# Kernel optimization log

Hardware: AMD Instinct MI355X
Metric: run time of the kernel (lower is better)

## Reference

```python
import jax, jax.numpy as jnp
import numpy as np

B, S, D, H = 16, 512, 512, 8
DH = D // H
EPS = 1e-5
NEG = -1.0e9


def _layernorm(v, g, b):
    mu = jnp.mean(v, axis=-1, keepdims=True)
    var = jnp.mean(jnp.square(v - mu), axis=-1, keepdims=True)
    return (v - mu) * jax.lax.rsqrt(var + EPS) * g + b


def setup_inputs() -> dict:
    key = jax.random.key(0)
    ks = jax.random.split(key, 12)
    sd = 1.0 / np.sqrt(D)
    return {
        "x": jax.random.normal(ks[0], (B, S, D), dtype=jnp.float32),
        "mask": jax.random.randint(ks[1], (B, S, S), 0, 2, dtype=jnp.int32),
        "ln_g": jnp.ones((D,), jnp.float32),
        "ln_b": jnp.zeros((D,), jnp.float32),
        "lna_g": jnp.ones((S,), jnp.float32),  # LayerNorm over attention scores (last dim = S = model_dim)
        "lna_b": jnp.zeros((S,), jnp.float32),
        "Wq": jax.random.uniform(ks[2], (D, D), jnp.float32, -sd, sd),
        "bq": jnp.zeros((D,), jnp.float32),
        "Wk": jax.random.uniform(ks[3], (D, D), jnp.float32, -sd, sd),
        "bk": jnp.zeros((D,), jnp.float32),
        "Wv": jax.random.uniform(ks[4], (D, D), jnp.float32, -sd, sd),
        "bv": jnp.zeros((D,), jnp.float32),
        "Wd": jax.random.uniform(ks[5], (D, D), jnp.float32, -sd, sd),
        "bd": jnp.zeros((D,), jnp.float32),
    }


def reference(x, mask, ln_g, ln_b, lna_g, lna_b, Wq, bq, Wk, bk, Wv, bv, Wd, bd):
    # pre-LN
    h = _layernorm(x, ln_g, ln_b)  # [B,S,D]
    # projections -> [B,H,S,DH]
    q = (h @ Wq + bq).reshape(B, S, H, DH).transpose(0, 2, 1, 3)
    k = (h @ Wk + bk).reshape(B, S, H, DH).transpose(0, 2, 1, 3)
    v = (h @ Wv + bv).reshape(B, S, H, DH).transpose(0, 2, 1, 3)
    # raw scores [B,H,S,S]
    scores = jnp.einsum("bhqd,bhkd->bhqk", q, k) / jnp.sqrt(jnp.asarray(DH, x.dtype))
    # non-standard: LayerNorm over the key axis of the score matrix
    scores = _layernorm(scores, lna_g, lna_b)
    # mask (broadcast over heads), then softmax
    scores = jnp.where(mask[:, None, :, :] == 0, jnp.asarray(NEG, x.dtype), scores)
    attn = jax.nn.softmax(scores, axis=-1)
    # dropout omitted (eval mode / deterministic reference)
    out = jnp.einsum("bhqk,bhkd->bhqd", attn, v)
    out = out.transpose(0, 2, 1, 3).reshape(B, S, D)
    out = out @ Wd + bd
    return out + x
```

## Files before the change

### kernel.cpp

```cpp
#include <hip/hip_runtime.h>
#include <hip/hip_bf16.h>
#include <stdint.h>


typedef __hip_bfloat16 bf16;
typedef __bf16 bf16x8 __attribute__((ext_vector_type(8)));
typedef float f32x4 __attribute__((ext_vector_type(4)));

#define MFMA16(a, b, c) __builtin_amdgcn_mfma_f32_16x16x32_bf16((a), (b), (c), 0, 0, 0)

static __device__ __forceinline__ bf16 f2b(float v) { return __float2bfloat16(v); }
static __device__ __forceinline__ bf16x8 ld8(const bf16* p) { return *(const bf16x8*)p; }
static __device__ __forceinline__ uint16_t f2bu(float v) {
  return __hip_bfloat16_raw(__float2bfloat16(v)).x;
}
static __device__ __forceinline__ float bu2f(uint32_t u) {
  union { uint32_t i; float f; } c;
  c.i = u << 16;
  return c.f;
}

__global__ __launch_bounds__(256) void transpose512(
    const float* __restrict__ W0, const float* __restrict__ W1,
    const float* __restrict__ W2, const float* __restrict__ W3,
    bf16* __restrict__ T0, bf16* __restrict__ T1,
    bf16* __restrict__ T2, bf16* __restrict__ T3) {
  __shared__ float t[32][33];
  const float* src; bf16* dst;
  switch (blockIdx.z) {
    case 0: src = W0; dst = T0; break;
    case 1: src = W1; dst = T1; break;
    case 2: src = W2; dst = T2; break;
    default: src = W3; dst = T3; break;
  }
  int tx = threadIdx.x, ty = threadIdx.y;
  int n0 = blockIdx.x * 32, k0 = blockIdx.y * 32;
#pragma unroll
  for (int i = 0; i < 4; i++) {
    int kk = ty * 4 + i;
    t[kk][tx] = src[(k0 + kk) * 512 + n0 + tx];
  }
  __syncthreads();
#pragma unroll
  for (int i = 0; i < 4; i++) {
    int nn = ty * 4 + i;
    dst[(n0 + nn) * 512 + k0 + tx] = f2b(t[tx][nn]);
  }
}

__global__ __launch_bounds__(256) void mask_pack(const int* __restrict__ mask,
                                                 uint32_t* __restrict__ bits) {
  size_t t = (size_t)blockIdx.x * 256 + threadIdx.x;
  int mv = mask[t];
  unsigned long long bal = __ballot(mv != 0);
  if ((threadIdx.x & 63) == 0) {
    ((unsigned long long*)bits)[t >> 6] = bal;
  }
}

__global__ __launch_bounds__(256) void mask_transpose(const uint32_t* __restrict__ bits,
                                                      uint32_t* __restrict__ tbits) {
  int t = blockIdx.x * 256 + threadIdx.x;
  int row = t >> 4, l = t & 15;
  const uint32_t* in = bits + row * 16;
  uint32_t o = 0;
#pragma unroll
  for (int jj = 0; jj < 32; jj++) {
    int key = l + 16 * jj;
    o |= ((in[key >> 5] >> (key & 31)) & 1u) << jj;
  }
  tbits[t] = o;
}

__global__ __launch_bounds__(256) void ln_rows(
    const float* __restrict__ x, const float* __restrict__ g,
    const float* __restrict__ be, bf16* __restrict__ h) {
  int row = blockIdx.x;
  int tid = threadIdx.x;
  const float* xr = x + (size_t)row * 512;
  float v0 = xr[tid], v1 = xr[tid + 256];
  float s = v0 + v1, s2 = v0 * v0 + v1 * v1;
#pragma unroll
  for (int m = 1; m < 64; m <<= 1) {
    s += __shfl_xor(s, m);
    s2 += __shfl_xor(s2, m);
  }
  __shared__ float rs[4], rs2[4];
  int w = tid >> 6;
  if ((tid & 63) == 0) { rs[w] = s; rs2[w] = s2; }
  __syncthreads();
  s = rs[0] + rs[1] + rs[2] + rs[3];
  s2 = rs2[0] + rs2[1] + rs2[2] + rs2[3];
  float mean = s * (1.0f / 512.0f);
  float var = s2 * (1.0f / 512.0f) - mean * mean;
  float rstd = rsqrtf(var + 1e-5f);
  bf16* hr = h + (size_t)row * 512;
  hr[tid] = f2b((v0 - mean) * rstd * g[tid] + be[tid]);
  hr[tid + 256] = f2b((v1 - mean) * rstd * g[tid + 256] + be[tid + 256]);
}

__global__ __launch_bounds__(256) void gemm_qkv(
    const bf16* __restrict__ hm,
    const bf16* __restrict__ WT0, const bf16* __restrict__ WT1, const bf16* __restrict__ WT2,
    const float* __restrict__ bq, const float* __restrict__ bk, const float* __restrict__ bv,
    bf16* __restrict__ outq, bf16* __restrict__ outk, bf16* __restrict__ outvT) {
  const int sel = blockIdx.z;
  const bf16* WT = sel == 0 ? WT0 : (sel == 1 ? WT1 : WT2);
  const float* bias = sel == 0 ? bq : (sel == 1 ? bk : bv);
  __shared__ __align__(16) bf16 As[128][40];
  __shared__ __align__(16) bf16 Bs[128][40];
  int tid = threadIdx.x;
  int w = tid >> 6, lane = tid & 63, q4 = lane >> 4, l16 = lane & 15;
  int wr = w >> 1, wc = w & 1;
  int m0 = blockIdx.x * 128, n0 = blockIdx.y * 128;
  f32x4 acc[4][4];
#pragma unroll
  for (int i = 0; i < 4; i++)
#pragma unroll
    for (int j = 0; j < 4; j++) acc[i][j] = (f32x4){0.f, 0.f, 0.f, 0.f};

  for (int kc = 0; kc < 16; kc++) {
    int k0 = kc * 32;
#pragma unroll
    for (int u = tid; u < 512; u += 256) {
      int row = u >> 2, c8 = (u & 3) * 8;
      *(bf16x8*)&As[row][c8] = ld8(&hm[(size_t)(m0 + row) * 512 + k0 + c8]);
      *(bf16x8*)&Bs[row][c8] = ld8(&WT[(size_t)(n0 + row) * 512 + k0 + c8]);
    }
    __syncthreads();
    bf16x8 af[4], bfr[4];
#pragma unroll
    for (int rt = 0; rt < 4; rt++) af[rt] = ld8(&As[wr * 64 + rt * 16 + l16][q4 * 8]);
#pragma unroll
    for (int nt = 0; nt < 4; nt++) bfr[nt] = ld8(&Bs[wc * 64 + nt * 16 + l16][q4 * 8]);
#pragma unroll
    for (int rt = 0; rt < 4; rt++)
#pragma unroll
      for (int nt = 0; nt < 4; nt++) acc[rt][nt] = MFMA16(af[rt], bfr[nt], acc[rt][nt]);
    __syncthreads();
  }

#pragma unroll
  for (int rt = 0; rt < 4; rt++) {
    int mbase = m0 + wr * 64 + rt * 16 + q4 * 4;
    int b = mbase >> 9, s0 = mbase & 511;
#pragma unroll
    for (int nt = 0; nt < 4; nt++) {
      int n = n0 + wc * 64 + nt * 16 + l16;
      float bsv = bias[n];
      int hh = n >> 6, dh = n & 63;
      if (sel == 2) {
        union { bf16 q[4]; uint2 u; } pk;
#pragma unroll
        for (int r = 0; r < 4; r++) pk.q[r] = f2b(acc[rt][nt][r] + bsv);
        *(uint2*)(outvT + ((size_t)((b * 8 + hh) * 64 + dh)) * 512 + s0) = pk.u;
      } else {
        bf16* dst = sel == 0 ? outq : outk;
        float scale = sel == 0 ? 0.125f : 1.0f;
#pragma unroll
        for (int r = 0; r < 4; r++)
          dst[((size_t)((b * 8 + hh) * 512 + s0 + r)) * 64 + dh] =
              f2b((acc[rt][nt][r] + bsv) * scale);
      }
    }
  }
}

__global__ __launch_bounds__(256, 2) void attn_fused(
    const bf16* __restrict__ q, const bf16* __restrict__ k, const bf16* __restrict__ vT,
    const uint32_t* __restrict__ tbits, const float* __restrict__ lg,
    const float* __restrict__ lb, bf16* __restrict__ ctx) {
  const int id = blockIdx.x;
  const int xcd = id & 7;
  const int j = id >> 3;
  const int mt = j & 7;
  const int bh = ((j >> 3) << 3) | xcd;
  const int m0 = mt * 64;
  const int b = bh >> 3, hh = bh & 7;
  const int tid = threadIdx.x;
  const int w = tid >> 6, lane = tid & 63, q4 = lane >> 4, l16 = lane & 15;

  __shared__ uint16_t ST[512][66];
  __shared__ __align__(16) bf16 SB[2][2560];

  const bf16* qb = q + ((size_t)bh * 512 + m0 + w * 16) * 64;
  const bf16* kb = k + (size_t)bh * 512 * 64;
  const bf16* vb = vT + (size_t)bh * 64 * 512;

  bf16x8 aq0 = ld8(qb + (size_t)l16 * 64 + q4 * 8);
  bf16x8 aq1 = ld8(qb + (size_t)l16 * 64 + 32 + q4 * 8);

  uint32_t tb[4];
#pragma unroll
  for (int r = 0; r < 4; r++)
    tb[r] = tbits[((size_t)b * 512 + m0 + w * 16 + q4 * 4 + r) * 16 + l16];

  const int col = w * 16 + q4 * 4;

  {
    int key0 = tid >> 3, dh8 = (tid & 7) * 8;
    *(bf16x8*)&SB[0][key0 * 72 + dh8] = ld8(kb + (size_t)key0 * 64 + dh8);
  }
  __syncthreads();

  float s[4] = {0.f, 0.f, 0.f, 0.f}, s2[4] = {0.f, 0.f, 0.f, 0.f};
  for (int c = 0; c < 16; c++) {
    const int buf = c & 1;
    if (c < 15) {
      int key0 = tid >> 3, dh8 = (tid & 7) * 8;
      *(bf16x8*)&SB[buf ^ 1][key0 * 72 + dh8] =
          ld8(kb + (size_t)((c + 1) * 32 + key0) * 64 + dh8);
    }
#pragma unroll
    for (int kg = 0; kg < 2; kg++) {
      const bf16* kp = &SB[buf][(kg * 16 + l16) * 72];
      bf16x8 b0 = ld8(kp + q4 * 8);
      bf16x8 b1 = ld8(kp + 32 + q4 * 8);
      f32x4 acc = (f32x4){0.f, 0.f, 0.f, 0.f};
      acc = MFMA16(aq0, b0, acc);
      acc = MFMA16(aq1, b1, acc);
#pragma unroll
      for (int r = 0; r < 4; r++) {
        float v = acc[r];
        s[r] += v;
        s2[r] += v * v;
      }
      int key = c * 32 + kg * 16 + l16;
      *(uint32_t*)&ST[key][col] = (uint32_t)f2bu(acc[0]) | ((uint32_t)f2bu(acc[1]) << 16);
      *(uint32_t*)&ST[key][col + 2] = (uint32_t)f2bu(acc[2]) | ((uint32_t)f2bu(acc[3]) << 16);
    }
    __syncthreads();
  }

  float mean[4], rstd[4];
#pragma unroll
  for (int r = 0; r < 4; r++) {
    float a = s[r], a2 = s2[r];
#pragma unroll
    for (int mm = 1; mm < 16; mm <<= 1) {
      a += __shfl_xor(a, mm);
      a2 += __shfl_xor(a2, mm);
    }
    float mu = a * (1.0f / 512.0f);
    float var = a2 * (1.0f / 512.0f) - mu * mu;
    mean[r] = mu;
    rstd[r] = rsqrtf(var + 1e-5f);
  }

  float se[4] = {0.f, 0.f, 0.f, 0.f};
#pragma unroll
  for (int i = 0; i < 32; i++) {
    int key = i * 16 + l16;
    float g = lg[key], be = lb[key];
    uint32_t d0 = *(uint32_t*)&ST[key][col];
    uint32_t d1 = *(uint32_t*)&ST[key][col + 2];
    float v[4] = {bu2f(d0 & 0xffff), bu2f(d0 >> 16), bu2f(d1 & 0xffff), bu2f(d1 >> 16)};
    uint16_t p[4];
#pragma unroll
    for (int r = 0; r < 4; r++) {
      float t = (v[r] - mean[r]) * rstd[r] * g + be;
      t = ((tb[r] >> i) & 1u) ? t : -1.0e9f;
      float pf = __expf(t);
      se[r] += pf;
      p[r] = f2bu(pf);
    }
    *(uint32_t*)&ST[key][col] = (uint32_t)p[0] | ((uint32_t)p[1] << 16);
    *(uint32_t*)&ST[key][col + 2] = (uint32_t)p[2] | ((uint32_t)p[3] << 16);
  }
  float inv[4];
#pragma unroll
  for (int r = 0; r < 4; r++) {
    float a = se[r];
#pragma unroll
    for (int mm = 1; mm < 16; mm <<= 1) a += __shfl_xor(a, mm);
    inv[r] = 1.0f / a;
  }

  {
    int dh = tid >> 2, kk8 = (tid & 3) * 8;
    *(bf16x8*)&SB[0][dh * 40 + kk8] = ld8(vb + (size_t)dh * 512 + kk8);
  }
  __syncthreads();

  f32x4 o[4];
#pragma unroll
  for (int nt = 0; nt < 4; nt++) o[nt] = (f32x4){0.f, 0.f, 0.f, 0.f};

  for (int c = 0; c < 16; c++) {
    const int buf = c & 1;
    if (c < 15) {
      int dh = tid >> 2, kk8 = (tid & 3) * 8;
      *(bf16x8*)&SB[buf ^ 1][dh * 40 + kk8] =
          ld8(vb + (size_t)dh * 512 + (c + 1) * 32 + kk8);
    }
    union { uint16_t u[8]; bf16x8 v; } af;
#pragma unroll
    for (int jj = 0; jj < 8; jj++) af.u[jj] = ST[c * 32 + q4 * 8 + jj][w * 16 + l16];
#pragma unroll
    for (int nt = 0; nt < 4; nt++) {
      bf16x8 bv8 = ld8(&SB[buf][(nt * 16 + l16) * 40 + q4 * 8]);
      o[nt] = MFMA16(af.v, bv8, o[nt]);
    }
    __syncthreads();
  }

  bf16* cb = ctx + ((size_t)b * 512 + m0 + w * 16) * 512 + hh * 64;
#pragma unroll
  for (int nt = 0; nt < 4; nt++)
#pragma unroll
    for (int r = 0; r < 4; r++)
      cb[(size_t)(q4 * 4 + r) * 512 + nt * 16 + l16] = f2b(o[nt][r] * inv[r]);
}

__global__ __launch_bounds__(256) void gemm_out(
    const bf16* __restrict__ ctx, const bf16* __restrict__ WT,
    const float* __restrict__ bd, const float* __restrict__ x, float* __restrict__ out) {
  __shared__ __align__(16) bf16 As[128][40];
  __shared__ __align__(16) bf16 Bs[128][40];
  int tid = threadIdx.x;
  int w = tid >> 6, lane = tid & 63, q4 = lane >> 4, l16 = lane & 15;
  int wr = w >> 1, wc = w & 1;
  int m0 = blockIdx.x * 128, n0 = blockIdx.y * 128;
  f32x4 acc[4][4];
#pragma unroll
  for (int i = 0; i < 4; i++)
#pragma unroll
    for (int j = 0; j < 4; j++) acc[i][j] = (f32x4){0.f, 0.f, 0.f, 0.f};

  for (int kc = 0; kc < 16; kc++) {
    int k0 = kc * 32;
#pragma unroll
    for (int u = tid; u < 512; u += 256) {
      int row = u >> 2, c8 = (u & 3) * 8;
      *(bf16x8*)&As[row][c8] = ld8(&ctx[(size_t)(m0 + row) * 512 + k0 + c8]);
      *(bf16x8*)&Bs[row][c8] = ld8(&WT[(size_t)(n0 + row) * 512 + k0 + c8]);
    }
    __syncthreads();
    bf16x8 af[4], bfr[4];
#pragma unroll
    for (int rt = 0; rt < 4; rt++) af[rt] = ld8(&As[wr * 64 + rt * 16 + l16][q4 * 8]);
#pragma unroll
    for (int nt = 0; nt < 4; nt++) bfr[nt] = ld8(&Bs[wc * 64 + nt * 16 + l16][q4 * 8]);
#pragma unroll
    for (int rt = 0; rt < 4; rt++)
#pragma unroll
      for (int nt = 0; nt < 4; nt++) acc[rt][nt] = MFMA16(af[rt], bfr[nt], acc[rt][nt]);
    __syncthreads();
  }
#pragma unroll
  for (int rt = 0; rt < 4; rt++) {
    int mbase = m0 + wr * 64 + rt * 16 + q4 * 4;
#pragma unroll
    for (int nt = 0; nt < 4; nt++) {
      int n = n0 + wc * 64 + nt * 16 + l16;
      float bsv = bd[n];
#pragma unroll
      for (int r = 0; r < 4; r++) {
        size_t idx = (size_t)(mbase + r) * 512 + n;
        out[idx] = acc[rt][nt][r] + bsv + x[idx];
      }
    }
  }
}

extern "C" void kernel_launch(void* const* d_in, const int* in_sizes, int n_in,
                              void* d_out, int out_size, void* d_ws, size_t ws_size,
                              hipStream_t stream) {
  const float* x = (const float*)d_in[0];
  const int* mask = (const int*)d_in[1];
  const float* ln_g = (const float*)d_in[2];
  const float* ln_b = (const float*)d_in[3];
  const float* lna_g = (const float*)d_in[4];
  const float* lna_b = (const float*)d_in[5];
  const float* Wq = (const float*)d_in[6];
  const float* bq = (const float*)d_in[7];
  const float* Wk = (const float*)d_in[8];
  const float* bk = (const float*)d_in[9];
  const float* Wv = (const float*)d_in[10];
  const float* bv = (const float*)d_in[11];
  const float* Wd = (const float*)d_in[12];
  const float* bd = (const float*)d_in[13];

  char* ws = (char*)d_ws;
  const size_t MB = 1024 * 1024;
  if (ws_size < 44 * MB) return;
  bf16* h = (bf16*)(ws);
  bf16* qd = (bf16*)(ws + 8 * MB);
  bf16* kd = (bf16*)(ws + 16 * MB);
  bf16* vTd = (bf16*)(ws + 24 * MB);
  bf16* ctx = (bf16*)(ws + 32 * MB);
  bf16* WqT = (bf16*)(ws + 40 * MB);
  bf16* WkT = (bf16*)(ws + 40 * MB + 512 * 1024);
  bf16* WvT = (bf16*)(ws + 40 * MB + 1024 * 1024);
  bf16* WdT = (bf16*)(ws + 40 * MB + 1536 * 1024);
  uint32_t* bits = (uint32_t*)(ws + 42 * MB);
  uint32_t* tbits = (uint32_t*)(ws + 42 * MB + 512 * 1024);

  transpose512<<<dim3(16, 16, 4), dim3(32, 8), 0, stream>>>(Wq, Wk, Wv, Wd, WqT, WkT, WvT, WdT);
  mask_pack<<<16384, 256, 0, stream>>>(mask, bits);
  mask_transpose<<<512, 256, 0, stream>>>(bits, tbits);
  ln_rows<<<8192, 256, 0, stream>>>(x, ln_g, ln_b, h);
  gemm_qkv<<<dim3(64, 4, 3), 256, 0, stream>>>(h, WqT, WkT, WvT, bq, bk, bv, qd, kd, vTd);
  attn_fused<<<1024, 256, 0, stream>>>(qd, kd, vTd, tbits, lna_g, lna_b, ctx);
  gemm_out<<<dim3(64, 4), 256, 0, stream>>>(ctx, WdT, bd, x, (float*)d_out);
}
```

Measured before the change: 205.0 us.

## Keep attention score tile in registers and shrink LDS to raise occupancy

The 512x64 bf16 score tile no longer lives in shared memory. Each thread now keeps its share of scores in 64 packed registers across the QK, LayerNorm/softmax and PV phases. For the PV MFMA, the A operand is transposed through a small per-wave scratch buffer guarded only by compiler fences. The LayerNorm gamma and beta vectors are staged in LDS, and the occupancy hint is raised to 3 blocks per CU. This removes most LDS traffic and footprint, but raises register pressure and risks spills. It also relies on intra-wave ordering of LDS accesses without a barrier.

```diff
diff --git a/kernel.cpp b/kernel.cpp
--- a/kernel.cpp
+++ b/kernel.cpp
@@ -8,6 +8,7 @@
 typedef float f32x4 __attribute__((ext_vector_type(4)));
 
 #define MFMA16(a, b, c) __builtin_amdgcn_mfma_f32_16x16x32_bf16((a), (b), (c), 0, 0, 0)
+#define WAVE_LDS_FENCE() asm volatile("" ::: "memory")
 
 static __device__ __forceinline__ bf16 f2b(float v) { return __float2bfloat16(v); }
 static __device__ __forceinline__ bf16x8 ld8(const bf16* p) { return *(const bf16x8*)p; }
@@ -166,7 +167,7 @@
   }
 }
 
-__global__ __launch_bounds__(256, 2) void attn_fused(
+__global__ __launch_bounds__(256, 3) void attn_fused(
     const bf16* __restrict__ q, const bf16* __restrict__ k, const bf16* __restrict__ vT,
     const uint32_t* __restrict__ tbits, const float* __restrict__ lg,
     const float* __restrict__ lb, bf16* __restrict__ ctx) {
@@ -180,8 +181,14 @@
   const int tid = threadIdx.x;
   const int w = tid >> 6, lane = tid & 63, q4 = lane >> 4, l16 = lane & 15;
 
-  __shared__ uint16_t ST[512][66];
   __shared__ __align__(16) bf16 SB[2][2560];
+  __shared__ uint16_t PBT[4][32][18];
+  __shared__ float SG[512], SBt[512];
+
+  SG[tid] = lg[tid];
+  SG[tid + 256] = lg[tid + 256];
+  SBt[tid] = lb[tid];
+  SBt[tid + 256] = lb[tid + 256];
 
   const bf16* qb = q + ((size_t)bh * 512 + m0 + w * 16) * 64;
   const bf16* kb = k + (size_t)bh * 512 * 64;
@@ -195,15 +202,15 @@
   for (int r = 0; r < 4; r++)
     tb[r] = tbits[((size_t)b * 512 + m0 + w * 16 + q4 * 4 + r) * 16 + l16];
 
-  const int col = w * 16 + q4 * 4;
-
   {
     int key0 = tid >> 3, dh8 = (tid & 7) * 8;
     *(bf16x8*)&SB[0][key0 * 72 + dh8] = ld8(kb + (size_t)key0 * 64 + dh8);
   }
   __syncthreads();
 
+  uint32_t sc[64];
   float s[4] = {0.f, 0.f, 0.f, 0.f}, s2[4] = {0.f, 0.f, 0.f, 0.f};
+#pragma unroll
   for (int c = 0; c < 16; c++) {
     const int buf = c & 1;
     if (c < 15) {
@@ -225,9 +232,8 @@
         s[r] += v;
         s2[r] += v * v;
       }
-      int key = c * 32 + kg * 16 + l16;
-      *(uint32_t*)&ST[key][col] = (uint32_t)f2bu(acc[0]) | ((uint32_t)f2bu(acc[1]) << 16);
-      *(uint32_t*)&ST[key][col + 2] = (uint32_t)f2bu(acc[2]) | ((uint32_t)f2bu(acc[3]) << 16);
+      sc[c * 4 + kg * 2] = (uint32_t)f2bu(acc[0]) | ((uint32_t)f2bu(acc[1]) << 16);
+      sc[c * 4 + kg * 2 + 1] = (uint32_t)f2bu(acc[2]) | ((uint32_t)f2bu(acc[3]) << 16);
     }
     __syncthreads();
   }
@@ -249,24 +255,26 @@
 
   float se[4] = {0.f, 0.f, 0.f, 0.f};
 #pragma unroll
-  for (int i = 0; i < 32; i++) {
-    int key = i * 16 + l16;
-    float g = lg[key], be = lb[key];
-    uint32_t d0 = *(uint32_t*)&ST[key][col];
-    uint32_t d1 = *(uint32_t*)&ST[key][col + 2];
-    float v[4] = {bu2f(d0 & 0xffff), bu2f(d0 >> 16), bu2f(d1 & 0xffff), bu2f(d1 >> 16)};
-    uint16_t p[4];
-#pragma unroll
-    for (int r = 0; r < 4; r++) {
-      float t = (v[r] - mean[r]) * rstd[r] * g + be;
-      t = ((tb[r] >> i) & 1u) ? t : -1.0e9f;
-      float pf = __expf(t);
-      se[r] += pf;
-      p[r] = f2bu(pf);
-    }
-    *(uint32_t*)&ST[key][col] = (uint32_t)p[0] | ((uint32_t)p[1] << 16);
-    *(uint32_t*)&ST[key][col + 2] = (uint32_t)p[2] | ((uint32_t)p[3] << 16);
-  }
+  for (int c = 0; c < 16; c++)
+#pragma unroll
+    for (int kg = 0; kg < 2; kg++) {
+      int key = c * 32 + kg * 16 + l16;
+      float g = SG[key], be = SBt[key];
+      int bit = 2 * c + kg;
+      uint32_t d0 = sc[c * 4 + kg * 2], d1 = sc[c * 4 + kg * 2 + 1];
+      float v[4] = {bu2f(d0 & 0xffff), bu2f(d0 >> 16), bu2f(d1 & 0xffff), bu2f(d1 >> 16)};
+      uint16_t p[4];
+#pragma unroll
+      for (int r = 0; r < 4; r++) {
+        float t = (v[r] - mean[r]) * rstd[r] * g + be;
+        t = ((tb[r] >> bit) & 1u) ? t : -1.0e9f;
+        float pf = __expf(t);
+        se[r] += pf;
+        p[r] = f2bu(pf);
+      }
+      sc[c * 4 + kg * 2] = (uint32_t)p[0] | ((uint32_t)p[1] << 16);
+      sc[c * 4 + kg * 2 + 1] = (uint32_t)p[2] | ((uint32_t)p[3] << 16);
+    }
   float inv[4];
 #pragma unroll
   for (int r = 0; r < 4; r++) {
@@ -286,6 +294,7 @@
 #pragma unroll
   for (int nt = 0; nt < 4; nt++) o[nt] = (f32x4){0.f, 0.f, 0.f, 0.f};
 
+#pragma unroll
   for (int c = 0; c < 16; c++) {
     const int buf = c & 1;
     if (c < 15) {
@@ -293,9 +302,15 @@
       *(bf16x8*)&SB[buf ^ 1][dh * 40 + kk8] =
           ld8(vb + (size_t)dh * 512 + (c + 1) * 32 + kk8);
     }
+    *(uint32_t*)&PBT[w][l16][q4 * 4] = sc[c * 4 + 0];
+    *(uint32_t*)&PBT[w][l16][q4 * 4 + 2] = sc[c * 4 + 1];
+    *(uint32_t*)&PBT[w][16 + l16][q4 * 4] = sc[c * 4 + 2];
+    *(uint32_t*)&PBT[w][16 + l16][q4 * 4 + 2] = sc[c * 4 + 3];
+    WAVE_LDS_FENCE();
     union { uint16_t u[8]; bf16x8 v; } af;
 #pragma unroll
-    for (int jj = 0; jj < 8; jj++) af.u[jj] = ST[c * 32 + q4 * 8 + jj][w * 16 + l16];
+    for (int jj = 0; jj < 8; jj++) af.u[jj] = PBT[w][q4 * 8 + jj][l16];
+    WAVE_LDS_FENCE();
 #pragma unroll
     for (int nt = 0; nt < 4; nt++) {
       bf16x8 bv8 = ld8(&SB[buf][(nt * 16 + l16) * 40 + q4 * 8]);
```

Result: slower. 233.4 us (+13.9%).

## Fuse mask packing into one kernel and stage GEMM tiles via direct global-to-LDS loads

Applied to the files above, without the earlier changes.

Merges the mask ballot-pack and bit-transpose kernels into a single kernel that reads the int mask directly and emits transposed bit words, removing one launch and an intermediate buffer. The QKV and output GEMMs now fill LDS with global_load_lds (direct global-to-LDS) instead of load-to-register then store, and drop the padded 40-column LDS rows for unpadded 32-column rows. The unpadded layout may bring back LDS bank conflicts on fragment reads. The new mask kernel uses a strided access pattern with only 512 blocks, which may coalesce poorly over the 16MB mask.

```diff
diff --git a/kernel.cpp b/kernel.cpp
--- a/kernel.cpp
+++ b/kernel.cpp
@@ -18,6 +18,11 @@
   union { uint32_t i; float f; } c;
   c.i = u << 16;
   return c.f;
+}
+static __device__ __forceinline__ void stage16(const bf16* g, bf16* l) {
+  __builtin_amdgcn_global_load_lds(
+      (const __attribute__((address_space(1))) void*)g,
+      (__attribute__((address_space(3))) void*)l, 16, 0, 0);
 }
 
 __global__ __launch_bounds__(256) void transpose512(
@@ -48,27 +53,14 @@
   }
 }
 
-__global__ __launch_bounds__(256) void mask_pack(const int* __restrict__ mask,
-                                                 uint32_t* __restrict__ bits) {
-  size_t t = (size_t)blockIdx.x * 256 + threadIdx.x;
-  int mv = mask[t];
-  unsigned long long bal = __ballot(mv != 0);
-  if ((threadIdx.x & 63) == 0) {
-    ((unsigned long long*)bits)[t >> 6] = bal;
-  }
-}
-
-__global__ __launch_bounds__(256) void mask_transpose(const uint32_t* __restrict__ bits,
-                                                      uint32_t* __restrict__ tbits) {
+__global__ __launch_bounds__(256) void mask_bits(const int* __restrict__ mask,
+                                                 uint32_t* __restrict__ tbits) {
   int t = blockIdx.x * 256 + threadIdx.x;
   int row = t >> 4, l = t & 15;
-  const uint32_t* in = bits + row * 16;
+  const int* mrow = mask + (size_t)row * 512 + l;
   uint32_t o = 0;
 #pragma unroll
-  for (int jj = 0; jj < 32; jj++) {
-    int key = l + 16 * jj;
-    o |= ((in[key >> 5] >> (key & 31)) & 1u) << jj;
-  }
+  for (int j = 0; j < 32; j++) o |= (mrow[j * 16] != 0 ? 1u : 0u) << j;
   tbits[t] = o;
 }
 
@@ -107,8 +99,8 @@
   const int sel = blockIdx.z;
   const bf16* WT = sel == 0 ? WT0 : (sel == 1 ? WT1 : WT2);
   const float* bias = sel == 0 ? bq : (sel == 1 ? bk : bv);
-  __shared__ __align__(16) bf16 As[128][40];
-  __shared__ __align__(16) bf16 Bs[128][40];
+  __shared__ __align__(16) bf16 As[128 * 32];
+  __shared__ __align__(16) bf16 Bs[128 * 32];
   int tid = threadIdx.x;
   int w = tid >> 6, lane = tid & 63, q4 = lane >> 4, l16 = lane & 15;
   int wr = w >> 1, wc = w & 1;
@@ -122,17 +114,20 @@
   for (int kc = 0; kc < 16; kc++) {
     int k0 = kc * 32;
 #pragma unroll
-    for (int u = tid; u < 512; u += 256) {
-      int row = u >> 2, c8 = (u & 3) * 8;
-      *(bf16x8*)&As[row][c8] = ld8(&hm[(size_t)(m0 + row) * 512 + k0 + c8]);
-      *(bf16x8*)&Bs[row][c8] = ld8(&WT[(size_t)(n0 + row) * 512 + k0 + c8]);
+    for (int u0 = 0; u0 < 2; u0++) {
+      int e = u0 * 256 + tid;
+      int row = e >> 2, c8 = (e & 3) * 8;
+      stage16(&hm[(size_t)(m0 + row) * 512 + k0 + c8], &As[e * 8]);
+      stage16(&WT[(size_t)(n0 + row) * 512 + k0 + c8], &Bs[e * 8]);
     }
     __syncthreads();
     bf16x8 af[4], bfr[4];
 #pragma unroll
-    for (int rt = 0; rt < 4; rt++) af[rt] = ld8(&As[wr * 64 + rt * 16 + l16][q4 * 8]);
-#pragma unroll
-    for (int nt = 0; nt < 4; nt++) bfr[nt] = ld8(&Bs[wc * 64 + nt * 16 + l16][q4 * 8]);
+    for (int rt = 0; rt < 4; rt++)
+      af[rt] = ld8(&As[(wr * 64 + rt * 16 + l16) * 32 + q4 * 8]);
+#pragma unroll
+    for (int nt = 0; nt < 4; nt++)
+      bfr[nt] = ld8(&Bs[(wc * 64 + nt * 16 + l16) * 32 + q4 * 8]);
 #pragma unroll
     for (int rt = 0; rt < 4; rt++)
 #pragma unroll
@@ -315,8 +310,8 @@
 __global__ __launch_bounds__(256) void gemm_out(
     const bf16* __restrict__ ctx, const bf16* __restrict__ WT,
     const float* __restrict__ bd, const float* __restrict__ x, float* __restrict__ out) {
-  __shared__ __align__(16) bf16 As[128][40];
-  __shared__ __align__(16) bf16 Bs[128][40];
+  __shared__ __align__(16) bf16 As[128 * 32];
+  __shared__ __align__(16) bf16 Bs[128 * 32];
   int tid = threadIdx.x;
   int w = tid >> 6, lane = tid & 63, q4 = lane >> 4, l16 = lane & 15;
   int wr = w >> 1, wc = w & 1;
@@ -330,17 +325,20 @@
   for (int kc = 0; kc < 16; kc++) {
     int k0 = kc * 32;
 #pragma unroll
-    for (int u = tid; u < 512; u += 256) {
-      int row = u >> 2, c8 = (u & 3) * 8;
-      *(bf16x8*)&As[row][c8] = ld8(&ctx[(size_t)(m0 + row) * 512 + k0 + c8]);
-      *(bf16x8*)&Bs[row][c8] = ld8(&WT[(size_t)(n0 + row) * 512 + k0 + c8]);
+    for (int u0 = 0; u0 < 2; u0++) {
+      int e = u0 * 256 + tid;
+      int row = e >> 2, c8 = (e & 3) * 8;
+      stage16(&ctx[(size_t)(m0 + row) * 512 + k0 + c8], &As[e * 8]);
+      stage16(&WT[(size_t)(n0 + row) * 512 + k0 + c8], &Bs[e * 8]);
     }
     __syncthreads();
     bf16x8 af[4], bfr[4];
 #pragma unroll
-    for (int rt = 0; rt < 4; rt++) af[rt] = ld8(&As[wr * 64 + rt * 16 + l16][q4 * 8]);
-#pragma unroll
-    for (int nt = 0; nt < 4; nt++) bfr[nt] = ld8(&Bs[wc * 64 + nt * 16 + l16][q4 * 8]);
+    for (int rt = 0; rt < 4; rt++)
+      af[rt] = ld8(&As[(wr * 64 + rt * 16 + l16) * 32 + q4 * 8]);
+#pragma unroll
+    for (int nt = 0; nt < 4; nt++)
+      bfr[nt] = ld8(&Bs[(wc * 64 + nt * 16 + l16) * 32 + q4 * 8]);
 #pragma unroll
     for (int rt = 0; rt < 4; rt++)
 #pragma unroll
@@ -393,12 +391,10 @@
   bf16* WkT = (bf16*)(ws + 40 * MB + 512 * 1024);
   bf16* WvT = (bf16*)(ws + 40 * MB + 1024 * 1024);
   bf16* WdT = (bf16*)(ws + 40 * MB + 1536 * 1024);
-  uint32_t* bits = (uint32_t*)(ws + 42 * MB);
-  uint32_t* tbits = (uint32_t*)(ws + 42 * MB + 512 * 1024);
+  uint32_t* tbits = (uint32_t*)(ws + 42 * MB);
 
   transpose512<<<dim3(16, 16, 4), dim3(32, 8), 0, stream>>>(Wq, Wk, Wv, Wd, WqT, WkT, WvT, WdT);
-  mask_pack<<<16384, 256, 0, stream>>>(mask, bits);
-  mask_transpose<<<512, 256, 0, stream>>>(bits, tbits);
+  mask_bits<<<512, 256, 0, stream>>>(mask, tbits);
   ln_rows<<<8192, 256, 0, stream>>>(x, ln_g, ln_b, h);
   gemm_qkv<<<dim3(64, 4, 3), 256, 0, stream>>>(h, WqT, WkT, WvT, bq, bk, bv, qd, kd, vTd);
   attn_fused<<<1024, 256, 0, stream>>>(qd, kd, vTd, tbits, lna_g, lna_b, ctx);
```

After: 191.9 us. 6.4% less time.
